# Performance work log

Measured on AMD Instinct MI355X. Metric: run time of the kernel, lower is better.

The kernel has to match this reference:

```python
import jax, jax.numpy as jnp
import numpy as np

HEADS = 16
WINDOW = 256
D_MODEL = 1024


def _ln(x, g, b, eps=1e-5):
    m = jnp.mean(x, -1, keepdims=True)
    var = jnp.mean((x - m) ** 2, -1, keepdims=True)
    return (x - m) * jax.lax.rsqrt(var + eps) * g + b


def _proj(x, g, b, W, bias):
    # torch: nn.Sequential(LayerNorm(d), Linear(d, h))
    return _ln(x, g, b) @ W.T + bias


def _bucket(x, pad_value):
    # x: (..., L, d) -> (..., nb, window, d), seq padded to multiple of window with pad_value
    L = x.shape[-2]
    n = WINDOW * (-(-L // WINDOW))
    pads = [(0, 0)] * x.ndim
    pads[-2] = (0, n - L)
    x = jnp.pad(x, pads, constant_values=pad_value)
    return x.reshape(*x.shape[:-2], n // WINDOW, WINDOW, x.shape[-1])


def _unfold(x, pad_value):
    # x: (..., nb, w, d) -> (..., nb, 2w, d): previous bucket (pad_value for bucket 0) || current
    pads = [(0, 0)] * x.ndim
    pads[-3] = (1, 0)
    prev = jnp.pad(x, pads, constant_values=pad_value)[..., :-1, :, :]
    return jnp.concatenate([prev, x], axis=-2)


def _rotary(x):
    # lucidrains rotary_embedding_torch default: theta=10000, interleaved pairs, positions 0..S-1 along dim -2
    S, d = x.shape[-2], x.shape[-1]
    inv = 1.0 / (10000.0 ** (jnp.arange(0, d, 2, dtype=jnp.float32) / d))
    freqs = jnp.arange(S, dtype=jnp.float32)[:, None] * inv[None, :]  # (S, d/2)
    freqs = jnp.repeat(freqs, 2, axis=-1)  # (S, d)
    cos, sin = jnp.cos(freqs).astype(x.dtype), jnp.sin(freqs).astype(x.dtype)
    xp = x.reshape(*x.shape[:-1], d // 2, 2)
    xr = jnp.stack([-xp[..., 1], xp[..., 0]], axis=-1).reshape(x.shape)
    return x * cos + xr * sin


def _forward(q, k, v, cell,
             ln_q_w, ln_q_b, w_q, b_q,
             ln_k_w, ln_k_b, w_k, b_k,
             ln_v_w, ln_v_b, w_v, b_v,
             ln_o_w, ln_o_b, w_o, b_o):
    B, L, D = q.shape
    hd = D // HEADS

    def split_heads(x):  # (B, L, D) -> (B, H, L, hd)
        return x.reshape(B, L, HEADS, hd).transpose(0, 2, 1, 3)

    qh = split_heads(_proj(q, ln_q_w, ln_q_b, w_q, b_q))
    kh = split_heads(_proj(k, ln_k_w, ln_k_b, w_k, b_k))
    vh = split_heads(_proj(v, ln_v_w, ln_v_b, w_v, b_v))

    bq = _bucket(qh, -1.0)                 # (B, H, nb, w, hd)
    bk = _unfold(_bucket(kh, -1.0), -1.0)  # (B, H, nb, 2w, hd)
    bv = _unfold(_bucket(vh, -1.0), -1.0)

    nb = bq.shape[2]
    n = nb * WINDOW
    i = _bucket(jnp.arange(n, dtype=jnp.int32)[:, None], -1)   # (nb, w, 1)
    j = jnp.swapaxes(_unfold(i, -1), -1, -2)                    # (nb, 1, 2w)
    mask = (i >= j) & (j != -1)                                 # (nb, w, 2w) causal + left pad
    req = _bucket(cell, -1)                                     # (B, 1, nb, w, 1)
    rek = jnp.swapaxes(_unfold(req, -1), -1, -2)                # (B, 1, nb, 1, 2w)
    mask = mask & (req == rek)                                  # (B, 1, nb, w, 2w)

    bq = _rotary(bq)
    bk = _rotary(bk)

    p = jnp.einsum('bhnqd,bhnkd->bhnqk', bq, bk) / jnp.sqrt(jnp.asarray(hd, bq.dtype))
    p = jnp.where(mask, p, jnp.finfo(p.dtype).min)
    a = jax.nn.softmax(p, axis=-1)
    o = jnp.einsum('bhnqk,bhnkd->bhnqd', a, bv)   # (B, H, nb, w, hd)
    o = o.reshape(B, HEADS, n, hd)[:, :, :L]      # drop seq padding
    o = o.transpose(0, 2, 1, 3).reshape(B, L, D)  # merge heads
    return _proj(o, ln_o_w, ln_o_b, w_o, b_o)


def setup_inputs() -> dict:
    key = jax.random.key(0)
    ks = jax.random.split(key, 10)
    B, L, D = 2, 4096, D_MODEL
    inp = {
        'q': jax.random.normal(ks[0], (B, L, D), dtype=jnp.float32),
        'k': jax.random.normal(ks[1], (B, L, D), dtype=jnp.float32),
        'v': jax.random.normal(ks[2], (B, L, D), dtype=jnp.float32),
        'cell': jnp.sort(jax.random.randint(ks[3], (B, 1, L, 1), 0, 64, dtype=jnp.int32), axis=2),
    }
    for idx, name in enumerate(['q', 'k', 'v', 'o']):
        inp[f'ln_{name}_w'] = jnp.ones((D,), jnp.float32)
        inp[f'ln_{name}_b'] = jnp.zeros((D,), jnp.float32)
        inp[f'w_{name}'] = jax.random.normal(ks[4 + idx], (D, D), dtype=jnp.float32) * 0.02
        inp[f'b_{name}'] = jnp.zeros((D,), jnp.float32)
    return inp


def reference(q, k, v, cell,
              ln_q_w, ln_q_b, w_q, b_q,
              ln_k_w, ln_k_b, w_k, b_k,
              ln_v_w, ln_v_b, w_v, b_v,
              ln_o_w, ln_o_b, w_o, b_o):
    return _forward(q, k, v, cell,
                    ln_q_w, ln_q_b, w_q, b_q,
                    ln_k_w, ln_k_b, w_k, b_k,
                    ln_v_w, ln_v_b, w_v, b_v,
                    ln_o_w, ln_o_b, w_o, b_o)
```

## Files before the change

### kernel.cpp

```cpp
#include <hip/hip_runtime.h>

#define HEADS 16
#define HD 64
#define DM 1024
#define LSEQ 4096
#define NEGF (-1.0e30f)

typedef __attribute__((ext_vector_type(8))) short bf16x8;
typedef __attribute__((ext_vector_type(4))) float f32x4;
typedef unsigned short u16;

#define MFMA16(a, b, c) __builtin_amdgcn_mfma_f32_16x16x32_bf16((a), (b), (c), 0, 0, 0)

static __device__ __forceinline__ float b2f(u16 u) {
  union { float f; unsigned i; } t; t.i = ((unsigned)u) << 16; return t.f;
}
static __device__ __forceinline__ u16 f2b(float f) {
  union { float f; unsigned i; } t; t.f = f;
  unsigned r = t.i + 0x7fffu + ((t.i >> 16) & 1u);
  return (u16)(r >> 16);
}
static __device__ __forceinline__ ushort4 pk4(float4 v) {
  return make_ushort4(f2b(v.x), f2b(v.y), f2b(v.z), f2b(v.w));
}
static __device__ __forceinline__ void gload16(const void* g, void* l) {
  __builtin_amdgcn_global_load_lds((const __attribute__((address_space(1))) void*)g,
                                   (__attribute__((address_space(3))) void*)l, 16, 0, 0);
}

__global__ __launch_bounds__(256) void prep(
    const float4* __restrict__ q, const float4* __restrict__ k, const float4* __restrict__ v,
    const float* __restrict__ g0, const float* __restrict__ b0,
    const float* __restrict__ g1, const float* __restrict__ b1,
    const float* __restrict__ g2, const float* __restrict__ b2,
    ushort4* __restrict__ o0, ushort4* __restrict__ o1, ushort4* __restrict__ o2,
    const float4* __restrict__ w0, const float4* __restrict__ w1,
    const float4* __restrict__ w2, const float4* __restrict__ w3,
    ushort4* __restrict__ wout,
    float* __restrict__ ropc, float* __restrict__ rops) {
  const int bid = blockIdx.x, tid = threadIdx.x;
  if (bid < 24576) {
    const int row = bid & 8191, sel = bid >> 13;
    const float4* src = (sel == 0) ? q : (sel == 1) ? k : v;
    const float* gam = (sel == 0) ? g0 : (sel == 1) ? g1 : g2;
    const float* bet = (sel == 0) ? b0 : (sel == 1) ? b1 : b2;
    ushort4* dst = (sel == 0) ? o0 : (sel == 1) ? o1 : o2;

    float4 v4 = src[(size_t)row * 256 + tid];
    float s = v4.x + v4.y + v4.z + v4.w;
    float s2 = v4.x * v4.x + v4.y * v4.y + v4.z * v4.z + v4.w * v4.w;
#pragma unroll
    for (int d = 1; d < 64; d <<= 1) { s += __shfl_xor(s, d); s2 += __shfl_xor(s2, d); }
    __shared__ float ps[8];
    int lane = tid & 63, wave = tid >> 6;
    if (lane == 0) { ps[wave] = s; ps[4 + wave] = s2; }
    __syncthreads();
    float tot = ps[0] + ps[1] + ps[2] + ps[3];
    float tot2 = ps[4] + ps[5] + ps[6] + ps[7];
    float mean = tot * (1.f / 1024.f);
    float var = tot2 * (1.f / 1024.f) - mean * mean;
    float rstd = rsqrtf(var + 1e-5f);
    float4 gv = ((const float4*)gam)[tid];
    float4 bv = ((const float4*)bet)[tid];
    dst[(size_t)row * 256 + tid] = make_ushort4(
        f2b((v4.x - mean) * rstd * gv.x + bv.x), f2b((v4.y - mean) * rstd * gv.y + bv.y),
        f2b((v4.z - mean) * rstd * gv.z + bv.z), f2b((v4.w - mean) * rstd * gv.w + bv.w));
  } else if (bid < 25600) {
    int i = (bid - 24576) * 256 + tid;
    wout[i]          = pk4(w0[i]);
    wout[i + 262144] = pk4(w1[i]);
    wout[i + 524288] = pk4(w2[i]);
    wout[i + 786432] = pk4(w3[i]);
  } else {
    int idx = (bid - 25600) * 256 + tid;
    int p = idx >> 6, d = idx & 63;
    int t2 = d & ~1;
    double inv = pow(10000.0, -(double)t2 / 64.0);
    double f = (double)p * inv;
    ropc[idx] = (float)cos(f);
    rops[idx] = (float)sin(f);
  }
}

__global__ __launch_bounds__(256) void ln_rows(const ushort4* __restrict__ xin,
                                               const float* __restrict__ gam,
                                               const float* __restrict__ bet,
                                               ushort4* __restrict__ out) {
  int row = blockIdx.x, tid = threadIdx.x;
  ushort4 u = xin[(size_t)row * 256 + tid];
  float4 v;
  v.x = b2f(u.x); v.y = b2f(u.y); v.z = b2f(u.z); v.w = b2f(u.w);
  float s = v.x + v.y + v.z + v.w;
  float s2 = v.x * v.x + v.y * v.y + v.z * v.z + v.w * v.w;
#pragma unroll
  for (int d = 1; d < 64; d <<= 1) { s += __shfl_xor(s, d); s2 += __shfl_xor(s2, d); }
  __shared__ float ps[8];
  int lane = tid & 63, wave = tid >> 6;
  if (lane == 0) { ps[wave] = s; ps[4 + wave] = s2; }
  __syncthreads();
  float tot = ps[0] + ps[1] + ps[2] + ps[3];
  float tot2 = ps[4] + ps[5] + ps[6] + ps[7];
  float mean = tot * (1.f / 1024.f);
  float var = tot2 * (1.f / 1024.f) - mean * mean;
  float rstd = rsqrtf(var + 1e-5f);
  float4 gv = ((const float4*)gam)[tid];
  float4 bv = ((const float4*)bet)[tid];
  out[(size_t)row * 256 + tid] = make_ushort4(
      f2b((v.x - mean) * rstd * gv.x + bv.x), f2b((v.y - mean) * rstd * gv.y + bv.y),
      f2b((v.z - mean) * rstd * gv.z + bv.z), f2b((v.w - mean) * rstd * gv.w + bv.w));
}

__global__ __launch_bounds__(256, 3) void gemm_qkv(
    const u16* __restrict__ Aq, const u16* __restrict__ Ak, const u16* __restrict__ Av,
    const u16* __restrict__ wbf,
    const float* __restrict__ bq, const float* __restrict__ bk, const float* __restrict__ bv,
    const float* __restrict__ ropc, const float* __restrict__ rops,
    u16* __restrict__ qrot, u16* __restrict__ krot, u16* __restrict__ vTp) {
  __shared__ __align__(16) char smem[34816];
  u16* Als = (u16*)smem;
  u16* Bls = (u16*)(smem + 16384);
  const int tid = threadIdx.x, lane = tid & 63, wave = tid >> 6;
  const int g = lane >> 4, ln15 = lane & 15;
  const int mode = blockIdx.y;
  const u16* A = (mode == 0) ? Aq : (mode == 1) ? Ak : Av;
  const u16* Bw = wbf + (size_t)mode * 1048576;
  const float* bias = (mode == 0) ? bq : (mode == 1) ? bk : bv;
  const int bid = blockIdx.x;
  const int xcd = bid & 7, idx = bid >> 3;
  const int row0 = (xcd * 8 + (idx >> 3)) * 128;
  const int col0 = (idx & 7) * 128;
  const int wm = (wave >> 1) * 64, wn = (wave & 1) * 64;
  const int K = 1024;
  f32x4 acc[4][4] = {};

  for (int k0 = 0; k0 < K; k0 += 64) {
#pragma unroll
    for (int i = 0; i < 4; ++i) {
      int ch = i * 4 + wave;
      int olin = ch * 1024 + lane * 16;
      int r = olin >> 7;
      int cel = ((olin ^ ((r & 7) << 4)) >> 1) & 63;
      gload16(A + (size_t)(row0 + r) * K + k0 + cel, (char*)Als + ch * 1024);
    }
#pragma unroll
    for (int i = 0; i < 4; ++i) {
      int ch = i * 4 + wave;
      int olin = ch * 1024 + lane * 16;
      int r = olin >> 7;
      int cel = ((olin ^ ((r & 7) << 4)) >> 1) & 63;
      gload16(Bw + (size_t)(col0 + r) * K + k0 + cel, (char*)Bls + ch * 1024);
    }
    __syncthreads();
#pragma unroll
    for (int ks = 0; ks < 2; ++ks) {
      bf16x8 af[4], bfv[4];
      int cb = (ks * 32 + g * 8) * 2;
#pragma unroll
      for (int mi = 0; mi < 4; ++mi) {
        int r = wm + mi * 16 + ln15;
        af[mi] = *(const bf16x8*)((const char*)Als + r * 128 + (cb ^ ((r & 7) << 4)));
      }
#pragma unroll
      for (int ni = 0; ni < 4; ++ni) {
        int r = wn + ni * 16 + ln15;
        bfv[ni] = *(const bf16x8*)((const char*)Bls + r * 128 + (cb ^ ((r & 7) << 4)));
      }
#pragma unroll
      for (int mi = 0; mi < 4; ++mi)
#pragma unroll
        for (int ni = 0; ni < 4; ++ni)
          acc[mi][ni] = MFMA16(af[mi], bfv[ni], acc[mi][ni]);
    }
    __syncthreads();
  }

  u16* Cl = (u16*)smem;
#pragma unroll
  for (int mi = 0; mi < 4; ++mi)
#pragma unroll
    for (int ni = 0; ni < 4; ++ni)
#pragma unroll
      for (int r = 0; r < 4; ++r) {
        int rowc = wm + mi * 16 + g * 4 + r;
        int colc = wn + ni * 16 + ln15;
        int row = row0 + rowc, col = col0 + colc;
        float val = acc[mi][ni][r] + bias[col];
        if (mode == 2) {
          Cl[colc * 136 + rowc] = f2b(val);
        } else {
          if (mode == 0) val *= 0.125f;
          float oth = __shfl_xor(val, 1);
          int d = col & 63;
          int pp = (row & 255) + ((mode == 1) ? 256 : 0);
          float cc = ropc[pp * 64 + d], ss = rops[pp * 64 + d];
          Cl[rowc * 136 + colc] = f2b((d & 1) ? (val * cc + oth * ss) : (val * cc - oth * ss));
        }
      }
  __syncthreads();
  if (mode == 2) {
#pragma unroll
    for (int i = 0; i < 8; ++i) {
      int c2 = i * 256 + tid;
      int dloc = c2 >> 4, lgrp = c2 & 15;
      bf16x8 vv = *(const bf16x8*)(Cl + dloc * 136 + lgrp * 8);
      int colg = col0 + dloc, hh = colg >> 6, d = colg & 63;
      int l = row0 + lgrp * 8, bb = l >> 12, ll = l & 4095;
      *(bf16x8*)(vTp + (((size_t)bb * HEADS + hh) * HD + d) * LSEQ + ll) = vv;
    }
  } else {
    u16* dst = (mode == 0) ? qrot : krot;
#pragma unroll
    for (int i = 0; i < 8; ++i) {
      int c2 = i * 256 + tid;
      int rowc = c2 >> 4, cgrp = c2 & 15;
      bf16x8 vv = *(const bf16x8*)(Cl + rowc * 136 + cgrp * 8);
      int l = row0 + rowc, bb = l >> 12, ll = l & 4095;
      int colg = col0 + cgrp * 8, hh = colg >> 6, d0 = colg & 63;
      *(bf16x8*)(dst + (((size_t)bb * HEADS + hh) * LSEQ + ll) * HD + d0) = vv;
    }
  }
}

__global__ __launch_bounds__(256, 3) void gemm_o(
    const u16* __restrict__ A, const u16* __restrict__ Bw, const float* __restrict__ bias,
    float* __restrict__ outf) {
  __shared__ __align__(16) u16 Als[128 * 64];
  __shared__ __align__(16) u16 Bls[128 * 64];
  const int tid = threadIdx.x, lane = tid & 63, wave = tid >> 6;
  const int g = lane >> 4, ln15 = lane & 15;
  const int bid = blockIdx.x;
  const int xcd = bid & 7, idx = bid >> 3;
  const int row0 = (xcd * 8 + (idx >> 3)) * 128;
  const int col0 = (idx & 7) * 128;
  const int wm = (wave >> 1) * 64, wn = (wave & 1) * 64;
  const int K = 1024, N = 1024;
  f32x4 acc[4][4] = {};

  for (int k0 = 0; k0 < K; k0 += 64) {
#pragma unroll
    for (int i = 0; i < 4; ++i) {
      int ch = i * 4 + wave;
      int olin = ch * 1024 + lane * 16;
      int r = olin >> 7;
      int cel = ((olin ^ ((r & 7) << 4)) >> 1) & 63;
      gload16(A + (size_t)(row0 + r) * K + k0 + cel, (char*)Als + ch * 1024);
    }
#pragma unroll
    for (int i = 0; i < 4; ++i) {
      int ch = i * 4 + wave;
      int olin = ch * 1024 + lane * 16;
      int r = olin >> 7;
      int cel = ((olin ^ ((r & 7) << 4)) >> 1) & 63;
      gload16(Bw + (size_t)(col0 + r) * K + k0 + cel, (char*)Bls + ch * 1024);
    }
    __syncthreads();
#pragma unroll
    for (int ks = 0; ks < 2; ++ks) {
      bf16x8 af[4], bfv[4];
      int cb = (ks * 32 + g * 8) * 2;
#pragma unroll
      for (int mi = 0; mi < 4; ++mi) {
        int r = wm + mi * 16 + ln15;
        af[mi] = *(const bf16x8*)((const char*)Als + r * 128 + (cb ^ ((r & 7) << 4)));
      }
#pragma unroll
      for (int ni = 0; ni < 4; ++ni) {
        int r = wn + ni * 16 + ln15;
        bfv[ni] = *(const bf16x8*)((const char*)Bls + r * 128 + (cb ^ ((r & 7) << 4)));
      }
#pragma unroll
      for (int mi = 0; mi < 4; ++mi)
#pragma unroll
        for (int ni = 0; ni < 4; ++ni)
          acc[mi][ni] = MFMA16(af[mi], bfv[ni], acc[mi][ni]);
    }
    __syncthreads();
  }

#pragma unroll
  for (int mi = 0; mi < 4; ++mi)
#pragma unroll
    for (int ni = 0; ni < 4; ++ni)
#pragma unroll
      for (int r = 0; r < 4; ++r) {
        int row = row0 + wm + mi * 16 + g * 4 + r;
        int col = col0 + wn + ni * 16 + ln15;
        outf[(size_t)row * N + col] = acc[mi][ni][r] + bias[col];
      }
}

__global__ __launch_bounds__(512, 2) void attn_kernel(
    const u16* __restrict__ qrot,
    const u16* __restrict__ krot,
    const u16* __restrict__ vT,
    const int* __restrict__ cell,
    const float* __restrict__ ropc, const float* __restrict__ rops,
    u16* __restrict__ o) {
  __shared__ __align__(16) u16 Kc[2][128 * 64];
  __shared__ __align__(16) u16 Pl[8 * 32 * 64];
  __shared__ int ci[256];
  __shared__ int cj[512];

  const int tid = threadIdx.x, lane = tid & 63, wave = tid >> 6;
  const int g = lane >> 4, ln15 = lane & 15;
  const int bucket = blockIdx.x & 15;
  const int h = (blockIdx.x >> 4) & 15;
  const int b = blockIdx.x >> 8;
  const int w0 = bucket * 256;
  const size_t base = (size_t)(b * HEADS + h) * LSEQ * HD;

  if (tid < 256) ci[tid] = cell[b * LSEQ + w0 + tid];
  {
    int gj = w0 - 256 + tid;
    cj[tid] = (gj >= 0) ? cell[b * LSEQ + gj] : (int)0x80000000;
  }

  bf16x8 qf[2][2];
#pragma unroll
  for (int mi = 0; mi < 2; ++mi)
#pragma unroll
    for (int ks = 0; ks < 2; ++ks)
      qf[mi][ks] = *(const bf16x8*)(qrot + base +
          (size_t)(w0 + wave * 32 + mi * 16 + ln15) * HD + ks * 32 + g * 8);

  bf16x8 qfB[2][2];
#pragma unroll
  for (int ks = 0; ks < 2; ++ks) {
    const int d0 = ks * 32 + g * 8;
    float rc[8], rs8[8];
#pragma unroll
    for (int j = 0; j < 8; ++j) {
      rc[j] = ropc[256 * 64 + d0 + j];
      rs8[j] = rops[256 * 64 + d0 + j];
    }
#pragma unroll
    for (int mi = 0; mi < 2; ++mi) {
      bf16x8 s = qf[mi][ks], t;
#pragma unroll
      for (int j = 0; j < 8; j += 2) {
        float e = b2f((u16)s[j]), od = b2f((u16)s[j + 1]);
        t[j]     = (short)f2b(e * rc[j] - od * rs8[j]);
        t[j + 1] = (short)f2b(e * rs8[j] + od * rc[j]);
      }
      qfB[mi][ks] = t;
    }
  }

  f32x4 Oa[2][4] = {};
  float mrow[2][4], lrow[2][4];
#pragma unroll
  for (int a1 = 0; a1 < 2; ++a1)
#pragma unroll
    for (int a2 = 0; a2 < 4; ++a2) { mrow[a1][a2] = NEGF; lrow[a1][a2] = 0.f; }

#define STAGE_K(bi, s)                                                          \
  {                                                                             \
    int gj0_ = w0 - 256 + (s) * 128;                                            \
    _Pragma("unroll")                                                           \
    for (int i_ = 0; i_ < 2; ++i_) {                                            \
      int ch_ = i_ * 8 + wave;                                                  \
      int olin_ = ch_ * 1024 + lane * 16;                                       \
      int r_ = olin_ >> 7;                                                      \
      int cel_ = ((olin_ ^ ((r_ & 7) << 4)) >> 1) & 63;                         \
      gload16(krot + base + (size_t)(gj0_ + r_) * HD + cel_,                    \
              (char*)Kc[bi] + ch_ * 1024);                                      \
    }                                                                           \
  }

  const int s0 = (bucket == 0) ? 2 : 0;
  STAGE_K(0, s0);
  __syncthreads();

  const int crb_lo = ci[0], crb_hi = ci[255];
  const int crw_lo = ci[wave * 32], crw_hi = ci[wave * 32 + 31];

  for (int s = s0; s < 4; ++s) {
    const int cur = (s - s0) & 1;
    if (s + 1 < 4) {
      int k1 = (s + 1) * 2;
      bool need = false;
#pragma unroll
      for (int kk = 0; kk < 2; ++kk) {
        int clo = cj[(k1 + kk) * 64], chi = cj[(k1 + kk) * 64 + 63];
        need = need || !(chi < crb_lo || clo > crb_hi);
      }
      if (need) STAGE_K(cur ^ 1, s + 1);
    }

#pragma unroll
    for (int sub = 0; sub < 2; ++sub) {
      const int k = s * 2 + sub;
      if (k * 64 > wave * 32 + 287) continue;
      {
        int clo = cj[k * 64], chi = cj[k * 64 + 63];
        if (chi < crw_lo || clo > crw_hi) continue;
      }
      const int gj0 = w0 - 256 + k * 64;
      const int lr0 = sub * 64;
      const bool prevhalf = (k < 4);

#pragma unroll
      for (int mi = 0; mi < 2; ++mi) {
        f32x4 sc[4] = {};
        __builtin_amdgcn_s_setprio(1);
#pragma unroll
        for (int ks = 0; ks < 2; ++ks) {
          int cb = (ks * 32 + g * 8) * 2;
          bf16x8 aq = prevhalf ? qfB[mi][ks] : qf[mi][ks];
#pragma unroll
          for (int ni = 0; ni < 4; ++ni) {
            int r = lr0 + ni * 16 + ln15;
            bf16x8 kf = *(const bf16x8*)((const char*)Kc[cur] + r * 128 + (cb ^ ((r & 7) << 4)));
            sc[ni] = MFMA16(aq, kf, sc[ni]);
          }
        }
        __builtin_amdgcn_s_setprio(0);
        float mx[4] = {NEGF, NEGF, NEGF, NEGF};
#pragma unroll
        for (int ni = 0; ni < 4; ++ni)
#pragma unroll
          for (int r = 0; r < 4; ++r) {
            int iloc = wave * 32 + mi * 16 + g * 4 + r;
            int p = k * 64 + ni * 16 + ln15;
            bool ok = (p <= iloc + 256) && (ci[iloc] == cj[p]);
            float sv = ok ? sc[ni][r] : NEGF;
            sc[ni][r] = sv;
            mx[r] = fmaxf(mx[r], sv);
          }
#pragma unroll
        for (int d = 1; d < 16; d <<= 1)
#pragma unroll
          for (int r = 0; r < 4; ++r) mx[r] = fmaxf(mx[r], __shfl_xor(mx[r], d));
        float rs[4] = {0.f, 0.f, 0.f, 0.f};
        bool big = false;
#pragma unroll
        for (int r = 0; r < 4; ++r) big = big || (mx[r] > mrow[mi][r] + 8.0f);
        if (__any(big)) {
#pragma unroll
          for (int r = 0; r < 4; ++r) {
            float mold = mrow[mi][r];
            float mnew = fmaxf(mold, mx[r]);
            float alpha = __expf(mold - mnew);
            mrow[mi][r] = mnew;
            lrow[mi][r] *= alpha;
#pragma unroll
            for (int nd = 0; nd < 4; ++nd) Oa[mi][nd][r] *= alpha;
          }
        }
#pragma unroll
        for (int ni = 0; ni < 4; ++ni)
#pragma unroll
          for (int r = 0; r < 4; ++r) {
            float sv = sc[ni][r];
            float p = (sv > NEGF * 0.5f) ? __expf(sv - mrow[mi][r]) : 0.f;
            rs[r] += p;
            int row = mi * 16 + g * 4 + r;
            int colb = (ni * 16 + ln15) * 2;
            *(u16*)((char*)Pl + wave * 4096 + row * 128 + (colb ^ ((row & 7) << 4))) = f2b(p);
          }
#pragma unroll
        for (int d = 1; d < 16; d <<= 1)
#pragma unroll
          for (int r = 0; r < 4; ++r) rs[r] += __shfl_xor(rs[r], d);
#pragma unroll
        for (int r = 0; r < 4; ++r) lrow[mi][r] += rs[r];
      }

#pragma unroll
      for (int jb = 0; jb < 2; ++jb) {
        bf16x8 pa[2], vb[4];
        int cb = (jb * 32 + g * 8) * 2;
#pragma unroll
        for (int mi = 0; mi < 2; ++mi) {
          int row = mi * 16 + ln15;
          pa[mi] = *(const bf16x8*)((const char*)Pl + wave * 4096 + row * 128 + (cb ^ ((row & 7) << 4)));
        }
#pragma unroll
        for (int nd = 0; nd < 4; ++nd) {
          int d = nd * 16 + ln15;
          int p0 = gj0 + jb * 32 + g * 8;
          vb[nd] = *(const bf16x8*)(vT + base + (size_t)d * LSEQ + p0);
        }
        __builtin_amdgcn_s_setprio(1);
#pragma unroll
        for (int mi = 0; mi < 2; ++mi)
#pragma unroll
          for (int nd = 0; nd < 4; ++nd) Oa[mi][nd] = MFMA16(pa[mi], vb[nd], Oa[mi][nd]);
        __builtin_amdgcn_s_setprio(0);
      }
    }

    __syncthreads();
  }

#pragma unroll
  for (int mi = 0; mi < 2; ++mi)
#pragma unroll
    for (int r = 0; r < 4; ++r) {
      float invl = 1.0f / lrow[mi][r];
      int gi = w0 + wave * 32 + mi * 16 + g * 4 + r;
      size_t ob = ((size_t)b * LSEQ + gi) * DM + h * HD;
#pragma unroll
      for (int nd = 0; nd < 4; ++nd) o[ob + nd * 16 + ln15] = f2b(Oa[mi][nd][r] * invl);
    }
#undef STAGE_K
}

extern "C" void kernel_launch(void* const* d_in, const int* in_sizes, int n_in,
                              void* d_out, int out_size, void* d_ws, size_t ws_size,
                              hipStream_t stream) {
  const float* q = (const float*)d_in[0];
  const float* k = (const float*)d_in[1];
  const float* v = (const float*)d_in[2];
  const int* cell = (const int*)d_in[3];
  const float* lnw[4] = {(const float*)d_in[4], (const float*)d_in[8], (const float*)d_in[12], (const float*)d_in[16]};
  const float* lnb[4] = {(const float*)d_in[5], (const float*)d_in[9], (const float*)d_in[13], (const float*)d_in[17]};
  const float* Wm[4]  = {(const float*)d_in[6], (const float*)d_in[10], (const float*)d_in[14], (const float*)d_in[18]};
  const float* bi[4]  = {(const float*)d_in[7], (const float*)d_in[11], (const float*)d_in[15], (const float*)d_in[19]};

  char* ws = (char*)d_ws;
  u16* xlnq  = (u16*)(ws);
  u16* wbf   = (u16*)(ws + 16777216);
  u16* qrot  = (u16*)(ws + 25165824);
  u16* krot  = (u16*)(ws + 41943040);
  u16* vT    = (u16*)(ws + 75497472);
  u16* obuf  = (u16*)(ws + 92274688);
  float* ropc = (float*)(ws + 109051904);
  float* rops = (float*)(ws + 109182976);
  u16* xlnk = obuf;
  u16* xlnv = (u16*)d_out;

  prep<<<25728, 256, 0, stream>>>(
      (const float4*)q, (const float4*)k, (const float4*)v,
      lnw[0], lnb[0], lnw[1], lnb[1], lnw[2], lnb[2],
      (ushort4*)xlnq, (ushort4*)xlnk, (ushort4*)xlnv,
      (const float4*)Wm[0], (const float4*)Wm[1], (const float4*)Wm[2], (const float4*)Wm[3],
      (ushort4*)wbf, ropc, rops);

  dim3 gq(512, 3);
  gemm_qkv<<<gq, 256, 0, stream>>>(xlnq, xlnk, xlnv, wbf, bi[0], bi[1], bi[2],
                                   ropc, rops, qrot, krot, vT);
  attn_kernel<<<512, 512, 0, stream>>>(qrot, krot, vT, cell, ropc, rops, obuf);
  ln_rows<<<8192, 256, 0, stream>>>((const ushort4*)obuf, lnw[3], lnb[3], (ushort4*)xlnq);
  gemm_o<<<512, 256, 0, stream>>>(xlnq, wbf + 3145728, bi[3], (float*)d_out);
}
```

Before: 194.0 us.

## Fold output LayerNorm into output GEMM epilogue via row stats and precomputed weight sums

The output LayerNorm is moved algebraically into the final projection. Gamma is folded into the bf16 weight, per-column sums W·gamma and W·beta+bias are precomputed in prep, and a small kernel computes only per-row mean and rstd. gemm_o then reads the raw attention output and applies rstd*acc - rstd*mean*c1 + c2b in its epilogue, which avoids writing and re-reading a normalized bf16 copy. The attention kernel also hoists its V-tile global loads ahead of the score computation to overlap their latency. This changes rounding, since the GEMM now runs on unnormalized bf16 values, and holding V in registers raises register pressure.

Result: no change. 191.4 us (median of 2 runs) (-1.3%).

```diff
diff --git a/kernel.cpp b/kernel.cpp
--- a/kernel.cpp
+++ b/kernel.cpp
@@ -37,8 +37,13 @@
     const float4* __restrict__ w0, const float4* __restrict__ w1,
     const float4* __restrict__ w2, const float4* __restrict__ w3,
     ushort4* __restrict__ wout,
-    float* __restrict__ ropc, float* __restrict__ rops) {
+    float* __restrict__ ropc, float* __restrict__ rops,
+    const float* __restrict__ g3, const float* __restrict__ b3,
+    const float* __restrict__ bias_o,
+    float* __restrict__ c1, float* __restrict__ c2b) {
+  __shared__ float ps[8];
   const int bid = blockIdx.x, tid = threadIdx.x;
+  const int lane = tid & 63, wave = tid >> 6;
   if (bid < 24576) {
     const int row = bid & 8191, sel = bid >> 13;
     const float4* src = (sel == 0) ? q : (sel == 1) ? k : v;
@@ -51,8 +56,6 @@
     float s2 = v4.x * v4.x + v4.y * v4.y + v4.z * v4.z + v4.w * v4.w;
 #pragma unroll
     for (int d = 1; d < 64; d <<= 1) { s += __shfl_xor(s, d); s2 += __shfl_xor(s2, d); }
-    __shared__ float ps[8];
-    int lane = tid & 63, wave = tid >> 6;
     if (lane == 0) { ps[wave] = s; ps[4 + wave] = s2; }
     __syncthreads();
     float tot = ps[0] + ps[1] + ps[2] + ps[3];
@@ -70,8 +73,11 @@
     wout[i]          = pk4(w0[i]);
     wout[i + 262144] = pk4(w1[i]);
     wout[i + 524288] = pk4(w2[i]);
-    wout[i + 786432] = pk4(w3[i]);
-  } else {
+    float4 wv = w3[i];
+    float4 g4 = ((const float4*)g3)[i & 255];
+    wv.x *= g4.x; wv.y *= g4.y; wv.z *= g4.z; wv.w *= g4.w;
+    wout[i + 786432] = pk4(wv);
+  } else if (bid < 25728) {
     int idx = (bid - 25600) * 256 + tid;
     int p = idx >> 6, d = idx & 63;
     int t2 = d & ~1;
@@ -79,35 +85,46 @@
     double f = (double)p * inv;
     ropc[idx] = (float)cos(f);
     rops[idx] = (float)sin(f);
-  }
-}
-
-__global__ __launch_bounds__(256) void ln_rows(const ushort4* __restrict__ xin,
-                                               const float* __restrict__ gam,
-                                               const float* __restrict__ bet,
-                                               ushort4* __restrict__ out) {
+  } else {
+    int n = bid - 25728;
+    float4 wv = w3[n * 256 + tid];
+    float4 gv = ((const float4*)g3)[tid];
+    float4 bv = ((const float4*)b3)[tid];
+    float s1 = wv.x * gv.x + wv.y * gv.y + wv.z * gv.z + wv.w * gv.w;
+    float s2 = wv.x * bv.x + wv.y * bv.y + wv.z * bv.z + wv.w * bv.w;
+#pragma unroll
+    for (int d = 1; d < 64; d <<= 1) { s1 += __shfl_xor(s1, d); s2 += __shfl_xor(s2, d); }
+    if (lane == 0) { ps[wave] = s1; ps[4 + wave] = s2; }
+    __syncthreads();
+    if (tid == 0) {
+      c1[n] = ps[0] + ps[1] + ps[2] + ps[3];
+      c2b[n] = ps[4] + ps[5] + ps[6] + ps[7] + bias_o[n];
+    }
+  }
+}
+
+__global__ __launch_bounds__(256) void ostats(const ushort4* __restrict__ xin,
+                                              float* __restrict__ mean,
+                                              float* __restrict__ rstd) {
+  __shared__ float ps[8];
   int row = blockIdx.x, tid = threadIdx.x;
+  int lane = tid & 63, wave = tid >> 6;
   ushort4 u = xin[(size_t)row * 256 + tid];
-  float4 v;
-  v.x = b2f(u.x); v.y = b2f(u.y); v.z = b2f(u.z); v.w = b2f(u.w);
-  float s = v.x + v.y + v.z + v.w;
-  float s2 = v.x * v.x + v.y * v.y + v.z * v.z + v.w * v.w;
+  float x = b2f(u.x), y = b2f(u.y), z = b2f(u.z), w = b2f(u.w);
+  float s = x + y + z + w;
+  float s2 = x * x + y * y + z * z + w * w;
 #pragma unroll
   for (int d = 1; d < 64; d <<= 1) { s += __shfl_xor(s, d); s2 += __shfl_xor(s2, d); }
-  __shared__ float ps[8];
-  int lane = tid & 63, wave = tid >> 6;
   if (lane == 0) { ps[wave] = s; ps[4 + wave] = s2; }
   __syncthreads();
-  float tot = ps[0] + ps[1] + ps[2] + ps[3];
-  float tot2 = ps[4] + ps[5] + ps[6] + ps[7];
-  float mean = tot * (1.f / 1024.f);
-  float var = tot2 * (1.f / 1024.f) - mean * mean;
-  float rstd = rsqrtf(var + 1e-5f);
-  float4 gv = ((const float4*)gam)[tid];
-  float4 bv = ((const float4*)bet)[tid];
-  out[(size_t)row * 256 + tid] = make_ushort4(
-      f2b((v.x - mean) * rstd * gv.x + bv.x), f2b((v.y - mean) * rstd * gv.y + bv.y),
-      f2b((v.z - mean) * rstd * gv.z + bv.z), f2b((v.w - mean) * rstd * gv.w + bv.w));
+  if (tid == 0) {
+    float tot = ps[0] + ps[1] + ps[2] + ps[3];
+    float tot2 = ps[4] + ps[5] + ps[6] + ps[7];
+    float m = tot * (1.f / 1024.f);
+    float var = tot2 * (1.f / 1024.f) - m * m;
+    mean[row] = m;
+    rstd[row] = rsqrtf(var + 1e-5f);
+  }
 }
 
 __global__ __launch_bounds__(256, 3) void gemm_qkv(
@@ -222,7 +239,9 @@
 }
 
 __global__ __launch_bounds__(256, 3) void gemm_o(
-    const u16* __restrict__ A, const u16* __restrict__ Bw, const float* __restrict__ bias,
+    const u16* __restrict__ A, const u16* __restrict__ Bw,
+    const float* __restrict__ mean, const float* __restrict__ rstd,
+    const float* __restrict__ c1, const float* __restrict__ c2b,
     float* __restrict__ outf) {
   __shared__ __align__(16) u16 Als[128 * 64];
   __shared__ __align__(16) u16 Bls[128 * 64];
@@ -280,13 +299,16 @@
 #pragma unroll
   for (int mi = 0; mi < 4; ++mi)
 #pragma unroll
-    for (int ni = 0; ni < 4; ++ni)
-#pragma unroll
-      for (int r = 0; r < 4; ++r) {
-        int row = row0 + wm + mi * 16 + g * 4 + r;
+    for (int r = 0; r < 4; ++r) {
+      int row = row0 + wm + mi * 16 + g * 4 + r;
+      float rho = rstd[row];
+      float rm = rho * mean[row];
+#pragma unroll
+      for (int ni = 0; ni < 4; ++ni) {
         int col = col0 + wn + ni * 16 + ln15;
-        outf[(size_t)row * N + col] = acc[mi][ni][r] + bias[col];
-      }
+        outf[(size_t)row * N + col] = rho * acc[mi][ni][r] - rm * c1[col] + c2b[col];
+      }
+    }
 }
 
 __global__ __launch_bounds__(512, 2) void attn_kernel(
@@ -399,6 +421,16 @@
       const int lr0 = sub * 64;
       const bool prevhalf = (k < 4);
 
+      bf16x8 vb[2][4];
+#pragma unroll
+      for (int jb = 0; jb < 2; ++jb)
+#pragma unroll
+        for (int nd = 0; nd < 4; ++nd) {
+          int d = nd * 16 + ln15;
+          int p0 = gj0 + jb * 32 + g * 8;
+          vb[jb][nd] = *(const bf16x8*)(vT + base + (size_t)d * LSEQ + p0);
+        }
+
 #pragma unroll
       for (int mi = 0; mi < 2; ++mi) {
         f32x4 sc[4] = {};
@@ -468,24 +500,18 @@
 
 #pragma unroll
       for (int jb = 0; jb < 2; ++jb) {
-        bf16x8 pa[2], vb[4];
+        bf16x8 pa[2];
         int cb = (jb * 32 + g * 8) * 2;
 #pragma unroll
         for (int mi = 0; mi < 2; ++mi) {
           int row = mi * 16 + ln15;
           pa[mi] = *(const bf16x8*)((const char*)Pl + wave * 4096 + row * 128 + (cb ^ ((row & 7) << 4)));
         }
-#pragma unroll
-        for (int nd = 0; nd < 4; ++nd) {
-          int d = nd * 16 + ln15;
-          int p0 = gj0 + jb * 32 + g * 8;
-          vb[nd] = *(const bf16x8*)(vT + base + (size_t)d * LSEQ + p0);
-        }
         __builtin_amdgcn_s_setprio(1);
 #pragma unroll
         for (int mi = 0; mi < 2; ++mi)
 #pragma unroll
-          for (int nd = 0; nd < 4; ++nd) Oa[mi][nd] = MFMA16(pa[mi], vb[nd], Oa[mi][nd]);
+          for (int nd = 0; nd < 4; ++nd) Oa[mi][nd] = MFMA16(pa[mi], vb[jb][nd], Oa[mi][nd]);
         __builtin_amdgcn_s_setprio(0);
       }
     }
@@ -523,6 +549,10 @@
   u16* wbf   = (u16*)(ws + 16777216);
   u16* qrot  = (u16*)(ws + 25165824);
   u16* krot  = (u16*)(ws + 41943040);
+  float* omean = (float*)(ws + 58720256);
+  float* orstd = (float*)(ws + 58753024);
+  float* c1    = (float*)(ws + 58785792);
+  float* c2b   = (float*)(ws + 58789888);
   u16* vT    = (u16*)(ws + 75497472);
   u16* obuf  = (u16*)(ws + 92274688);
   float* ropc = (float*)(ws + 109051904);
@@ -530,17 +560,18 @@
   u16* xlnk = obuf;
   u16* xlnv = (u16*)d_out;
 
-  prep<<<25728, 256, 0, stream>>>(
+  prep<<<26752, 256, 0, stream>>>(
       (const float4*)q, (const float4*)k, (const float4*)v,
       lnw[0], lnb[0], lnw[1], lnb[1], lnw[2], lnb[2],
       (ushort4*)xlnq, (ushort4*)xlnk, (ushort4*)xlnv,
       (const float4*)Wm[0], (const float4*)Wm[1], (const float4*)Wm[2], (const float4*)Wm[3],
-      (ushort4*)wbf, ropc, rops);
+      (ushort4*)wbf, ropc, rops,
+      lnw[3], lnb[3], bi[3], c1, c2b);
 
   dim3 gq(512, 3);
   gemm_qkv<<<gq, 256, 0, stream>>>(xlnq, xlnk, xlnv, wbf, bi[0], bi[1], bi[2],
                                    ropc, rops, qrot, krot, vT);
   attn_kernel<<<512, 512, 0, stream>>>(qrot, krot, vT, cell, ropc, rops, obuf);
-  ln_rows<<<8192, 256, 0, stream>>>((const ushort4*)obuf, lnw[3], lnb[3], (ushort4*)xlnq);
-  gemm_o<<<512, 256, 0, stream>>>(xlnq, wbf + 3145728, bi[3], (float*)d_out);
-}
+  ostats<<<8192, 256, 0, stream>>>((const ushort4*)obuf, omean, orstd);
+  gemm_o<<<512, 256, 0, stream>>>(obuf, wbf + 3145728, omean, orstd, c1, c2b, (float*)d_out);
+}
```
